# Kernel optimization log

Hardware: AMD Instinct MI355X
Metric: run time of the kernel (lower is better)

The kernel has to match this reference:

```python
import jax, jax.numpy as jnp
import numpy as np


def setup_inputs() -> dict:
    key = jax.random.key(0)
    k1, k2 = jax.random.split(key)
    B, C = 128, 256
    kernel = jax.random.normal(k1, (B, C, 8, 8), dtype=jnp.float32)
    search = jax.random.normal(k2, (B, C, 32, 32), dtype=jnp.float32)
    return {"kernel": kernel, "search": search}


def reference(kernel, search):
    # Faithful xcorr_depthwise: per-(batch, channel) 2D cross-correlation,
    # expressed as a grouped conv with groups = B*C (same trick as pysot).
    B, C, hk, wk = kernel.shape
    _, _, Hs, Ws = search.shape
    x = search.reshape(1, B * C, Hs, Ws)          # NCHW, single "image"
    w = kernel.reshape(B * C, 1, hk, wk)          # OIHW, one filter per group
    out = jax.lax.conv_general_dilated(
        x, w,
        window_strides=(1, 1),
        padding="VALID",
        feature_group_count=B * C,
        dimension_numbers=("NCHW", "OIHW", "NCHW"),
    )
    Ho, Wo = Hs - hk + 1, Ws - wk + 1
    return out.reshape(B, C, Ho, Wo)
```

## Files before the change

kernel.cpp:

```cpp
#include <hip/hip_runtime.h>

#define BLOCK 256
#define CHPB  8
#define SROW  33
#define SCH   (32 * SROW)

__global__ __launch_bounds__(BLOCK, 4) void dwxcorr_kernel(
    const float* __restrict__ kern,
    const float* __restrict__ srch,
    float* __restrict__ out,
    int nch)
{
    __shared__ float s_s[CHPB * SCH];
    __shared__ float s_k[CHPB * 64];

    const int tid = threadIdx.x;
    const int ch0 = blockIdx.x * CHPB;

    {
        const float4* g = (const float4*)(srch + (size_t)ch0 * 1024);
        #pragma unroll
        for (int it = 0; it < 8; ++it) {
            int e4 = tid + it * BLOCK;
            int ch = e4 >> 8;
            if (ch0 + ch < nch) {
                float4 v = g[e4];
                int rem = e4 & 255;
                int r   = rem >> 3;
                int c   = rem & 7;
                float* dst = &s_s[ch * SCH + r * SROW + c * 4];
                dst[0] = v.x; dst[1] = v.y; dst[2] = v.z; dst[3] = v.w;
            }
        }
    }
    if (tid < CHPB * 16) {
        int ch = tid >> 4;
        if (ch0 + ch < nch) {
            const float4* g = (const float4*)(kern + (size_t)ch0 * 64);
            ((float4*)s_k)[tid] = g[tid];
        }
    }
    __syncthreads();

    const int wave = tid >> 6;
    const int lane = tid & 63;
    const int ch_l = wave * 2 + (lane >> 5);
    const int j    = lane & 31;

    if (j < 25 && ch0 + ch_l < nch) {
        float kk[64];
        const float4* kb = (const float4*)&s_k[ch_l * 64];
        #pragma unroll
        for (int w = 0; w < 16; ++w) {
            float4 kv = kb[w];
            kk[w*4+0] = kv.x; kk[w*4+1] = kv.y; kk[w*4+2] = kv.z; kk[w*4+3] = kv.w;
        }

        float acc[25];
        #pragma unroll
        for (int i = 0; i < 25; ++i) acc[i] = 0.0f;

        const float* sb = &s_s[ch_l * SCH + j];

        #pragma unroll
        for (int r = 0; r < 32; ++r) {
            float sv[8];
            #pragma unroll
            for (int v = 0; v < 8; ++v) sv[v] = sb[r * SROW + v];

            #pragma unroll
            for (int u = 0; u < 8; ++u) {
                if (u >= ((r > 24) ? (r - 24) : 0) && u <= ((r < 7) ? r : 7)) {
                    const int i = r - u;
                    #pragma unroll
                    for (int v = 0; v < 8; ++v)
                        acc[i] = fmaf(kk[u*8 + v], sv[v], acc[i]);
                }
            }
        }

        float* op = out + (size_t)(ch0 + ch_l) * 625 + j;
        #pragma unroll
        for (int i = 0; i < 25; ++i) op[i * 25] = acc[i];
    }
}

extern "C" void kernel_launch(void* const* d_in, const int* in_sizes, int n_in,
                              void* d_out, int out_size, void* d_ws, size_t ws_size,
                              hipStream_t stream) {
    const float* kern = (const float*)d_in[0];
    const float* srch = (const float*)d_in[1];
    float* out = (float*)d_out;

    const int nch = in_sizes[0] / 64;
    const int grid = (nch + CHPB - 1) / CHPB;
    dwxcorr_kernel<<<grid, BLOCK, 0, stream>>>(kern, srch, out, nch);
}
```

Baseline: 57.00 us.

## Double-buffer channel groups with async global-to-LDS loads in persistent blocks

Each block now handles 8 groups of 8 channels and stages the next group into a second LDS buffer with global_load_lds while computing the current one. Waits use manual vmcnt counts. The padded LDS row stride is dropped because direct-to-LDS loads need a contiguous layout. The goal is to hide global load latency behind FMA work. In exchange, grid size and occupancy drop (launch bounds 2), unpadded rows may cause LDS bank conflicts, and the vmcnt counts overlap with the output stores, so the waits may be miscounted. Bounds checks on nch are also removed.

```diff
diff --git a/kernel.cpp b/kernel.cpp
--- a/kernel.cpp
+++ b/kernel.cpp
@@ -1,88 +1,119 @@
 #include <hip/hip_runtime.h>
+#include <stdint.h>
 
-#define BLOCK 256
-#define CHPB  8
-#define SROW  33
-#define SCH   (32 * SROW)
+#define BLOCK  256
+#define NW     4
+#define CHPG   8
+#define NG     8
+#define SB_CH  1024
+#define SBUF_G (CHPG * SB_CH)
+#define KBUF_G (CHPG * 64)
 
-__global__ __launch_bounds__(BLOCK, 4) void dwxcorr_kernel(
-    const float* __restrict__ kern,
-    const float* __restrict__ srch,
-    float* __restrict__ out,
-    int nch)
+__device__ __forceinline__ void gl_lds16(const float* g, float* l) {
+    __builtin_amdgcn_global_load_lds(
+        (__attribute__((address_space(1))) void*)(uintptr_t)g,
+        (__attribute__((address_space(3))) void*)l, 16, 0, 0);
+}
+__device__ __forceinline__ void gl_lds4(const float* g, float* l) {
+    __builtin_amdgcn_global_load_lds(
+        (__attribute__((address_space(1))) void*)(uintptr_t)g,
+        (__attribute__((address_space(3))) void*)l, 4, 0, 0);
+}
+
+__device__ __forceinline__ void stage_group(
+    const float* __restrict__ srch, const float* __restrict__ kern,
+    float* s_s, float* s_k, int cg, int w, int lane, int p)
 {
-    __shared__ float s_s[CHPB * SCH];
-    __shared__ float s_k[CHPB * 64];
+    const int cA = cg + 2 * w;
+    const float* gs = srch + (size_t)cA * SB_CH;
+    float* ls = s_s + p * SBUF_G + w * 2048;
+    #pragma unroll
+    for (int t = 0; t < 8; ++t)
+        gl_lds16(gs + t * 256 + lane * 4, ls + t * 256);
+    const float* gk = kern + (size_t)cA * 64;
+    float* lk = s_k + p * KBUF_G + w * 128;
+    #pragma unroll
+    for (int t = 0; t < 2; ++t)
+        gl_lds4(gk + t * 64 + lane, lk + t * 64);
+}
 
-    const int tid = threadIdx.x;
-    const int ch0 = blockIdx.x * CHPB;
+__device__ __forceinline__ void compute_group(
+    const float* s_s, const float* s_k, float* __restrict__ out,
+    int cg, int w, int lane, int p, bool act)
+{
+    const int h  = lane >> 5;
+    const int j  = lane & 31;
+    const int ch = cg + 2 * w + h;
+    const float* sb = s_s + p * SBUF_G + w * 2048 + h * SB_CH + j;
+    const float* kb = s_k + p * KBUF_G + w * 128 + h * 64;
 
-    {
-        const float4* g = (const float4*)(srch + (size_t)ch0 * 1024);
+    if (act) {
+        float kk[64];
         #pragma unroll
-        for (int it = 0; it < 8; ++it) {
-            int e4 = tid + it * BLOCK;
-            int ch = e4 >> 8;
-            if (ch0 + ch < nch) {
-                float4 v = g[e4];
-                int rem = e4 & 255;
-                int r   = rem >> 3;
-                int c   = rem & 7;
-                float* dst = &s_s[ch * SCH + r * SROW + c * 4];
-                dst[0] = v.x; dst[1] = v.y; dst[2] = v.z; dst[3] = v.w;
-            }
+        for (int t = 0; t < 16; ++t) {
+            float4 kv = ((const float4*)kb)[t];
+            kk[4*t+0] = kv.x; kk[4*t+1] = kv.y; kk[4*t+2] = kv.z; kk[4*t+3] = kv.w;
         }
-    }
-    if (tid < CHPB * 16) {
-        int ch = tid >> 4;
-        if (ch0 + ch < nch) {
-            const float4* g = (const float4*)(kern + (size_t)ch0 * 64);
-            ((float4*)s_k)[tid] = g[tid];
-        }
-    }
-    __syncthreads();
-
-    const int wave = tid >> 6;
-    const int lane = tid & 63;
-    const int ch_l = wave * 2 + (lane >> 5);
-    const int j    = lane & 31;
-
-    if (j < 25 && ch0 + ch_l < nch) {
-        float kk[64];
-        const float4* kb = (const float4*)&s_k[ch_l * 64];
-        #pragma unroll
-        for (int w = 0; w < 16; ++w) {
-            float4 kv = kb[w];
-            kk[w*4+0] = kv.x; kk[w*4+1] = kv.y; kk[w*4+2] = kv.z; kk[w*4+3] = kv.w;
-        }
-
         float acc[25];
         #pragma unroll
         for (int i = 0; i < 25; ++i) acc[i] = 0.0f;
-
-        const float* sb = &s_s[ch_l * SCH + j];
 
         #pragma unroll
         for (int r = 0; r < 32; ++r) {
             float sv[8];
             #pragma unroll
-            for (int v = 0; v < 8; ++v) sv[v] = sb[r * SROW + v];
-
+            for (int v = 0; v < 8; ++v) sv[v] = sb[r * 32 + v];
+            const int lo = (r > 24) ? (r - 24) : 0;
+            const int hi = (r < 7) ? r : 7;
             #pragma unroll
             for (int u = 0; u < 8; ++u) {
-                if (u >= ((r > 24) ? (r - 24) : 0) && u <= ((r < 7) ? r : 7)) {
-                    const int i = r - u;
+                if (u >= lo && u <= hi) {
                     #pragma unroll
                     for (int v = 0; v < 8; ++v)
-                        acc[i] = fmaf(kk[u*8 + v], sv[v], acc[i]);
+                        acc[r - u] = fmaf(kk[u * 8 + v], sv[v], acc[r - u]);
                 }
             }
         }
-
-        float* op = out + (size_t)(ch0 + ch_l) * 625 + j;
+        float* op = out + (size_t)ch * 625 + j;
         #pragma unroll
         for (int i = 0; i < 25; ++i) op[i * 25] = acc[i];
     }
+}
+
+#define WAITV(N) do { \
+    asm volatile("s_waitcnt vmcnt(" #N ")" ::: "memory"); \
+    __builtin_amdgcn_sched_barrier(0); \
+} while (0)
+
+__global__ __launch_bounds__(BLOCK, 2) void dwxcorr_kernel(
+    const float* __restrict__ kern,
+    const float* __restrict__ srch,
+    float* __restrict__ out)
+{
+    __shared__ float s_s[2 * SBUF_G];
+    __shared__ float s_k[2 * KBUF_G];
+
+    const int tid  = threadIdx.x;
+    const int w    = tid >> 6;
+    const int lane = tid & 63;
+    const bool act = ((lane & 31) < 25);
+    const int c0   = blockIdx.x * (CHPG * NG);
+
+    stage_group(srch, kern, s_s, s_k, c0, w, lane, 0);
+
+    stage_group(srch, kern, s_s, s_k, c0 + CHPG, w, lane, 1);
+    WAITV(10);
+    compute_group(s_s, s_k, out, c0, w, lane, 0, act);
+
+    #pragma unroll 1
+    for (int g = 1; g <= NG - 2; ++g) {
+        stage_group(srch, kern, s_s, s_k, c0 + (g + 1) * CHPG, w, lane, (g + 1) & 1);
+        WAITV(35);
+        compute_group(s_s, s_k, out, c0 + g * CHPG, w, lane, g & 1, act);
+    }
+
+    WAITV(25);
+    compute_group(s_s, s_k, out, c0 + (NG - 1) * CHPG, w, lane, (NG - 1) & 1, act);
 }
 
 extern "C" void kernel_launch(void* const* d_in, const int* in_sizes, int n_in,
@@ -92,7 +123,7 @@
     const float* srch = (const float*)d_in[1];
     float* out = (float*)d_out;
 
-    const int nch = in_sizes[0] / 64;
-    const int grid = (nch + CHPB - 1) / CHPB;
-    dwxcorr_kernel<<<grid, BLOCK, 0, stream>>>(kern, srch, out, nch);
+    const int nch  = in_sizes[0] / 64;
+    const int grid = nch / (CHPG * NG);
+    dwxcorr_kernel<<<grid, BLOCK, 0, stream>>>(kern, srch, out);
 }
```

Result: slower. 58.45 us (+2.5%).
